# Kernel tuning notes

Hardware: AMD Instinct MI355X
Metric: run time of the kernel (lower is better)

## Reference

```python
import jax, jax.numpy as jnp
import numpy as np

DIM = 1024
FF = 4096
E = 8
K = 2


def setup_inputs() -> dict:
    key = jax.random.key(0)
    ks = jax.random.split(key, 6)
    x = jax.random.normal(ks[0], (4, 2048, DIM), dtype=jnp.float32)
    wr = jax.random.normal(ks[1], (E, DIM), dtype=jnp.float32) * 0.02   # router weight [E, D]
    w1 = jax.random.normal(ks[2], (E, DIM, 2 * FF), dtype=jnp.float32) * 0.02  # SwiGLU in-proj
    b1 = jax.random.normal(ks[3], (E, 2 * FF), dtype=jnp.float32) * 0.02
    w2 = jax.random.normal(ks[4], (E, FF, DIM), dtype=jnp.float32) * 0.02  # SwiGLU out-proj
    b2 = jax.random.normal(ks[5], (E, DIM), dtype=jnp.float32) * 0.02
    return {"x": x, "wr": wr, "w1": w1, "b1": b1, "w2": w2, "b2": b2}


def reference(x, wr, w1, b1, w2, b2):
    B, T, D = x.shape
    n_experts = wr.shape[0]
    xf = x.reshape(B * T, D)                      # [N, D]
    logits = xf @ wr.T                            # [N, E]
    topk_vals, topk_idx = jax.lax.top_k(logits, K)  # [N, K]
    gates = jax.nn.softmax(topk_vals, axis=-1)      # [N, K]
    out = jnp.zeros_like(xf)
    for e in range(n_experts):
        # combined gate weight for tokens routed to expert e (0 otherwise)
        g_e = jnp.sum(jnp.where(topk_idx == e, gates, 0.0), axis=-1)  # [N]
        u = xf @ w1[e] + b1[e]                    # [N, 2F]
        a, b = jnp.split(u, 2, axis=-1)
        h = jax.nn.silu(a) * b                    # SwiGLU
        y_e = h @ w2[e] + b2[e]                   # [N, D]
        out = out + g_e[:, None] * y_e
    return out.reshape(B, T, D)
```

## Files before the change

kernel.cpp:

```cpp
#include <hip/hip_runtime.h>

#define NE 8
#define NTOK 8192
#define NDIM 1024
#define NFF 4096

typedef short bf16x8 __attribute__((ext_vector_type(8)));
typedef float f32x4 __attribute__((ext_vector_type(4)));
typedef unsigned short us_t;
typedef us_t us4 __attribute__((ext_vector_type(4)));
typedef us_t us8 __attribute__((ext_vector_type(8)));

#define MFMA16 __builtin_amdgcn_mfma_f32_16x16x32_bf16

__device__ __forceinline__ us_t f2bf(float f) {
  unsigned int u = __float_as_uint(f);
  u += 0x7fffu + ((u >> 16) & 1u);
  return (us_t)(u >> 16);
}

__device__ __forceinline__ void gload16(const void* g, void* l) {
  __builtin_amdgcn_global_load_lds(
      (const __attribute__((address_space(1))) void*)g,
      (__attribute__((address_space(3))) void*)l, 16, 0, 0);
}

__global__ __launch_bounds__(256) void router_kernel(
    const float* __restrict__ x, const float* __restrict__ wr,
    int* __restrict__ counts, int* __restrict__ tok_list,
    int4* __restrict__ tok4, float2* __restrict__ gate2,
    us_t* __restrict__ xbf)
{
  __shared__ float wr_s[NE * NDIM];
  int tid = threadIdx.x;
#pragma unroll
  for (int i = 0; i < 8; ++i)
    ((float4*)wr_s)[tid + 256 * i] = ((const float4*)wr)[tid + 256 * i];
  __syncthreads();
  int w = tid >> 6, l = tid & 63;
  int t = blockIdx.x * 4 + w;
  float4 xv[4];
#pragma unroll
  for (int j = 0; j < 4; ++j) xv[j] = ((const float4*)x)[(size_t)t * 256 + j * 64 + l];
#pragma unroll
  for (int j = 0; j < 4; ++j) {
    us4 o;
    o.x = f2bf(xv[j].x); o.y = f2bf(xv[j].y); o.z = f2bf(xv[j].z); o.w = f2bf(xv[j].w);
    ((us4*)xbf)[(size_t)t * 256 + j * 64 + l] = o;
  }
  float logits[NE];
#pragma unroll
  for (int e = 0; e < NE; ++e) {
    float p = 0.f;
#pragma unroll
    for (int j = 0; j < 4; ++j) {
      float4 wv = ((const float4*)wr_s)[e * 256 + j * 64 + l];
      p += xv[j].x * wv.x + xv[j].y * wv.y + xv[j].z * wv.z + xv[j].w * wv.w;
    }
#pragma unroll
    for (int s = 32; s > 0; s >>= 1) p += __shfl_xor(p, s, 64);
    logits[e] = p;
  }
  if (l == 0) {
    int e1 = 0; float v1 = logits[0];
#pragma unroll
    for (int e = 1; e < NE; ++e) if (logits[e] > v1) { v1 = logits[e]; e1 = e; }
    int e2 = -1; float v2 = -3.4e38f;
#pragma unroll
    for (int e = 0; e < NE; ++e) if (e != e1 && logits[e] > v2) { v2 = logits[e]; e2 = e; }
    float ge = expf(v2 - v1);
    float g1 = 1.f / (1.f + ge);
    float g2 = 1.f - g1;
    int i1 = atomicAdd(&counts[e1], 1);
    tok_list[e1 * NTOK + i1] = t;
    int i2 = atomicAdd(&counts[e2], 1);
    tok_list[e2 * NTOK + i2] = t;
    tok4[t] = make_int4(e1, i1, e2, i2);
    gate2[t] = make_float2(g1, g2);
  }
}

__global__ void prefix8(const int* __restrict__ counts, int* __restrict__ offsets) {
  if (threadIdx.x == 0) {
    int s = 0;
    for (int e = 0; e < NE; ++e) { offsets[e] = s; s += counts[e]; }
  }
}

__global__ __launch_bounds__(256) void transpose_cvt(
    const float* __restrict__ in, us_t* __restrict__ out, int R, int C)
{
  __shared__ float tile[64][65];
  int e = blockIdx.z;
  const float* ip = in + (size_t)e * R * C;
  us_t* op = out + (size_t)e * R * C;
  int r0 = blockIdx.y * 64, c0 = blockIdx.x * 64;
  int tid = threadIdx.x;
#pragma unroll
  for (int q = 0; q < 4; ++q) {
    int id = tid + 256 * q;
    int rr = id >> 4, c4 = id & 15;
    float4 v = *(const float4*)&ip[(size_t)(r0 + rr) * C + c0 + c4 * 4];
    tile[rr][c4 * 4 + 0] = v.x; tile[rr][c4 * 4 + 1] = v.y;
    tile[rr][c4 * 4 + 2] = v.z; tile[rr][c4 * 4 + 3] = v.w;
  }
  __syncthreads();
#pragma unroll
  for (int q = 0; q < 2; ++q) {
    int id = tid + 256 * q;
    int cc = id >> 3, r8 = id & 7;
    us8 o;
#pragma unroll
    for (int j = 0; j < 8; ++j) o[j] = f2bf(tile[r8 * 8 + j][cc]);
    *(us8*)&op[(size_t)(c0 + cc) * R + r0 + r8 * 8] = o;
  }
}

__global__ __launch_bounds__(256) void gemm1_swiglu(
    const us_t* __restrict__ xbf,
    const us_t* __restrict__ w1T,
    const float* __restrict__ b1,
    const int* __restrict__ counts, const int* __restrict__ offsets,
    const int* __restrict__ tok_list,
    us_t* __restrict__ hbuf)
{
  const int e = blockIdx.z, mt = blockIdx.y, ct = blockIdx.x;
  const int cnt = counts[e];
  if (mt * 128 >= cnt) return;
  const int off = offsets[e];
  const int tid = threadIdx.x, w = tid >> 6, l = tid & 63;
  const int wr_ = w >> 1, wc = w & 1;

  __shared__ char ldsA[16384];
  __shared__ char ldsB[32768];
  __shared__ int tok_l[128];

  if (tid < 128) {
    int r = mt * 128 + tid;
    tok_l[tid] = tok_list[e * NTOK + (r < cnt ? r : cnt - 1)];
  }
  __syncthreads();

  f32x4 zf = {0.f, 0.f, 0.f, 0.f};
  f32x4 acc[2][4][4];
#pragma unroll
  for (int h_ = 0; h_ < 2; ++h_)
#pragma unroll
    for (int cg = 0; cg < 4; ++cg)
#pragma unroll
      for (int rg = 0; rg < 4; ++rg) acc[h_][cg][rg] = zf;

  const size_t w1base = (size_t)e * 2 * NFF * NDIM;

  for (int kt = 0; kt < NDIM; kt += 64) {
    __syncthreads();
#pragma unroll
    for (int i = 0; i < 12; ++i) {
      int c = w + i * 4;
      const us_t* gsrc; char* ldst;
      if (c < 16) {
        int p = c * 1024 + l * 16;
        int row = p >> 7;
        int ir = (p & 127) ^ ((row & 7) << 4);
        gsrc = xbf + (size_t)tok_l[row] * NDIM + kt + (ir >> 1);
        ldst = ldsA + c * 1024;
      } else {
        int cb = c - 16;
        int p = cb * 1024 + l * 16;
        int row = p >> 7;
        int ir = (p & 127) ^ ((row & 7) << 4);
        int ncol = (row < 128) ? (ct * 128 + row) : (NFF + ct * 128 + row - 128);
        gsrc = w1T + w1base + (size_t)ncol * NDIM + kt + (ir >> 1);
        ldst = ldsB + cb * 1024;
      }
      gload16(gsrc, ldst);
    }
    __syncthreads();
#pragma unroll
    for (int ks = 0; ks < 2; ++ks) {
      bf16x8 af[4];
#pragma unroll
      for (int rg = 0; rg < 4; ++rg) {
        int row = wr_ * 64 + rg * 16 + (l & 15);
        int ir = (ks * 64 + (l >> 4) * 16) ^ ((row & 7) << 4);
        af[rg] = *(const bf16x8*)(ldsA + row * 128 + ir);
      }
#pragma unroll
      for (int h_ = 0; h_ < 2; ++h_)
#pragma unroll
        for (int cg = 0; cg < 4; ++cg) {
          int crow = h_ * 128 + wc * 64 + cg * 16 + (l & 15);
          int ir = (ks * 64 + (l >> 4) * 16) ^ ((crow & 7) << 4);
          bf16x8 bfr = *(const bf16x8*)(ldsB + crow * 128 + ir);
#pragma unroll
          for (int rg = 0; rg < 4; ++rg)
            acc[h_][cg][rg] = MFMA16(af[rg], bfr, acc[h_][cg][rg], 0, 0, 0);
        }
    }
  }

  float b1a[4], b1b[4];
#pragma unroll
  for (int cg = 0; cg < 4; ++cg) {
    int n_a = ct * 128 + wc * 64 + cg * 16 + (l & 15);
    b1a[cg] = b1[e * 2 * NFF + n_a];
    b1b[cg] = b1[e * 2 * NFF + NFF + n_a];
  }
#pragma unroll
  for (int cg = 0; cg < 4; ++cg) {
    int n_a = ct * 128 + wc * 64 + cg * 16 + (l & 15);
#pragma unroll
    for (int rg = 0; rg < 4; ++rg) {
#pragma unroll
      for (int j = 0; j < 4; ++j) {
        int rt = wr_ * 64 + rg * 16 + (l >> 4) * 4 + j;
        int r = mt * 128 + rt;
        if (r < cnt) {
          float a = acc[0][cg][rg][j] + b1a[cg];
          float b = acc[1][cg][rg][j] + b1b[cg];
          float hv = (a / (1.f + __expf(-a))) * b;
          hbuf[(size_t)(off + r) * NFF + n_a] = f2bf(hv);
        }
      }
    }
  }
}

__global__ __launch_bounds__(256) void gemm2_slot(
    const us_t* __restrict__ hbuf,
    const us_t* __restrict__ w2T,
    const float* __restrict__ b2,
    const int* __restrict__ counts, const int* __restrict__ offsets,
    float* __restrict__ ybuf)
{
  const int b = blockIdx.x;
  const int xcd = b & 7, k = b >> 3;
  const int mt = k & 63;
  const int combo = xcd + 8 * (k >> 6);
  const int nt = combo & 7, e = combo >> 3;

  const int cnt = counts[e];
  if (mt * 128 >= cnt) return;
  const int off = offsets[e];
  const int tid = threadIdx.x, w = tid >> 6, l = tid & 63;
  const int wr_ = w >> 1, wc = w & 1;

  __shared__ char ldsA[16384];
  __shared__ char ldsB[16384];

  unsigned int soff[8];
#pragma unroll
  for (int i = 0; i < 8; ++i) {
    int c = w + i * 4;
    if (i < 4) {
      int p = c * 1024 + l * 16;
      int row = p >> 7;
      int ir = (p & 127) ^ ((row & 7) << 4);
      int r = mt * 128 + row; if (r >= cnt) r = cnt - 1;
      soff[i] = (unsigned int)((off + r) * (NFF * 2) + ir);
    } else {
      int cb = c - 16;
      int p = cb * 1024 + l * 16;
      int row = p >> 7;
      int ir = (p & 127) ^ ((row & 7) << 4);
      soff[i] = (unsigned int)((nt * 128 + row) * (NFF * 2) + ir);
    }
  }

  f32x4 zf = {0.f, 0.f, 0.f, 0.f};
  f32x4 acc[4][4];
#pragma unroll
  for (int cg = 0; cg < 4; ++cg)
#pragma unroll
    for (int rg = 0; rg < 4; ++rg) acc[cg][rg] = zf;

  const char* hB = (const char*)hbuf;
  const char* wB = (const char*)w2T + (size_t)e * NDIM * NFF * 2;

  for (int ktb = 0; ktb < NFF * 2; ktb += 128) {
    __syncthreads();
#pragma unroll
    for (int i = 0; i < 4; ++i)
      gload16(hB + soff[i] + ktb, ldsA + (w + i * 4) * 1024);
#pragma unroll
    for (int i = 4; i < 8; ++i)
      gload16(wB + soff[i] + ktb, ldsB + (w + i * 4 - 16) * 1024);
    __syncthreads();
#pragma unroll
    for (int ks = 0; ks < 2; ++ks) {
      bf16x8 af[4];
#pragma unroll
      for (int rg = 0; rg < 4; ++rg) {
        int row = wr_ * 64 + rg * 16 + (l & 15);
        int ir = (ks * 64 + (l >> 4) * 16) ^ ((row & 7) << 4);
        af[rg] = *(const bf16x8*)(ldsA + row * 128 + ir);
      }
#pragma unroll
      for (int cg = 0; cg < 4; ++cg) {
        int crow = wc * 64 + cg * 16 + (l & 15);
        int ir = (ks * 64 + (l >> 4) * 16) ^ ((crow & 7) << 4);
        bf16x8 bfr = *(const bf16x8*)(ldsB + crow * 128 + ir);
#pragma unroll
        for (int rg = 0; rg < 4; ++rg)
          acc[cg][rg] = MFMA16(af[rg], bfr, acc[cg][rg], 0, 0, 0);
      }
    }
  }

#pragma unroll
  for (int cg = 0; cg < 4; ++cg) {
    int col = nt * 128 + wc * 64 + cg * 16 + (l & 15);
    float b2v = b2[e * NDIM + col];
#pragma unroll
    for (int rg = 0; rg < 4; ++rg) {
#pragma unroll
      for (int j = 0; j < 4; ++j) {
        int rt = wr_ * 64 + rg * 16 + (l >> 4) * 4 + j;
        int r = mt * 128 + rt;
        if (r < cnt)
          ybuf[(size_t)(off + r) * NDIM + col] = acc[cg][rg][j] + b2v;
      }
    }
  }
}

__global__ __launch_bounds__(256) void combine_kernel(
    const float* __restrict__ ybuf, const int* __restrict__ offsets,
    const int4* __restrict__ tok4, const float2* __restrict__ gate2,
    float* __restrict__ out)
{
  int t = blockIdx.x;
  int4 p = tok4[t];
  float2 g = gate2[t];
  int s1 = offsets[p.x] + p.y;
  int s2 = offsets[p.z] + p.w;
  const float4* y1 = (const float4*)(ybuf + (size_t)s1 * NDIM);
  const float4* y2 = (const float4*)(ybuf + (size_t)s2 * NDIM);
  float4 a = y1[threadIdx.x];
  float4 b = y2[threadIdx.x];
  float4 o;
  o.x = g.x * a.x + g.y * b.x;
  o.y = g.x * a.y + g.y * b.y;
  o.z = g.x * a.z + g.y * b.z;
  o.w = g.x * a.w + g.y * b.w;
  ((float4*)(out + (size_t)t * NDIM))[threadIdx.x] = o;
}

extern "C" void kernel_launch(void* const* d_in, const int* in_sizes, int n_in,
                              void* d_out, int out_size, void* d_ws, size_t ws_size,
                              hipStream_t stream) {
  const float* x  = (const float*)d_in[0];
  const float* wr = (const float*)d_in[1];
  const float* w1 = (const float*)d_in[2];
  const float* b1 = (const float*)d_in[3];
  const float* w2 = (const float*)d_in[4];
  const float* b2 = (const float*)d_in[5];
  float* out = (float*)d_out;
  char* ws = (char*)d_ws;

  int*    counts   = (int*)(ws + 0);
  int*    offsets  = (int*)(ws + 256);
  int*    tok_list = (int*)(ws + 512);
  int4*   tok4     = (int4*)(ws + 512 + 262144);
  float2* gate2    = (float2*)(ws + 512 + 262144 + 131072);
  us_t*   xbf      = (us_t*)(ws + 524800);
  us_t*   hbuf     = (us_t*)(ws + 524800 + (size_t)NTOK * NDIM * 2);
  us_t*   wT       = (us_t*)(ws + 524800 + (size_t)NTOK * NDIM * 2
                                          + (size_t)2 * NTOK * NFF * 2);
  float*  ybuf     = (float*)((char*)wT + 67108864);

  hipMemsetAsync(counts, 0, 32, stream);

  router_kernel<<<NTOK / 4, 256, 0, stream>>>(x, wr, counts, tok_list, tok4, gate2, xbf);
  prefix8<<<1, 64, 0, stream>>>(counts, offsets);

  transpose_cvt<<<dim3(2 * NFF / 64, NDIM / 64, NE), 256, 0, stream>>>(w1, wT, NDIM, 2 * NFF);
  gemm1_swiglu<<<dim3(NFF / 128, NTOK / 128, NE), 256, 0, stream>>>(
      xbf, wT, b1, counts, offsets, tok_list, hbuf);

  transpose_cvt<<<dim3(NDIM / 64, NFF / 64, NE), 256, 0, stream>>>(w2, wT, NFF, NDIM);
  gemm2_slot<<<4096, 256, 0, stream>>>(
      hbuf, wT, b2, counts, offsets, ybuf);

  combine_kernel<<<NTOK, 256, 0, stream>>>(ybuf, offsets, tok4, gate2, out);
}
```

Measured before the change: 958.2 us.

## Split gemm2 K dimension in two with atomic accumulation and move bias to combine

Splits the second expert GEMM along the FF reduction dimension into two halves, doubling the grid and accumulating partial results into ybuf with float atomicAdd. ybuf is zeroed with a memset beforehand, and the b2 bias add moves into the combine kernel. The aim is more parallel blocks for better CU occupancy, at the cost of a large memset, atomic write traffic and nondeterministic summation order.

```diff
diff --git a/kernel.cpp b/kernel.cpp
--- a/kernel.cpp
+++ b/kernel.cpp
@@ -229,7 +229,6 @@
 __global__ __launch_bounds__(256) void gemm2_slot(
     const us_t* __restrict__ hbuf,
     const us_t* __restrict__ w2T,
-    const float* __restrict__ b2,
     const int* __restrict__ counts, const int* __restrict__ offsets,
     float* __restrict__ ybuf)
 {
@@ -237,7 +236,9 @@
   const int xcd = b & 7, k = b >> 3;
   const int mt = k & 63;
   const int combo = xcd + 8 * (k >> 6);
-  const int nt = combo & 7, e = combo >> 3;
+  const int nt = combo & 7;
+  const int ks = (combo >> 3) & 1;
+  const int e = combo >> 4;
 
   const int cnt = counts[e];
   if (mt * 128 >= cnt) return;
@@ -277,7 +278,8 @@
   const char* hB = (const char*)hbuf;
   const char* wB = (const char*)w2T + (size_t)e * NDIM * NFF * 2;
 
-  for (int ktb = 0; ktb < NFF * 2; ktb += 128) {
+  const int ktb0 = ks * 4096;
+  for (int ktb = ktb0; ktb < ktb0 + 4096; ktb += 128) {
     __syncthreads();
 #pragma unroll
     for (int i = 0; i < 4; ++i)
@@ -287,18 +289,18 @@
       gload16(wB + soff[i] + ktb, ldsB + (w + i * 4 - 16) * 1024);
     __syncthreads();
 #pragma unroll
-    for (int ks = 0; ks < 2; ++ks) {
+    for (int ks2 = 0; ks2 < 2; ++ks2) {
       bf16x8 af[4];
 #pragma unroll
       for (int rg = 0; rg < 4; ++rg) {
         int row = wr_ * 64 + rg * 16 + (l & 15);
-        int ir = (ks * 64 + (l >> 4) * 16) ^ ((row & 7) << 4);
+        int ir = (ks2 * 64 + (l >> 4) * 16) ^ ((row & 7) << 4);
         af[rg] = *(const bf16x8*)(ldsA + row * 128 + ir);
       }
 #pragma unroll
       for (int cg = 0; cg < 4; ++cg) {
         int crow = wc * 64 + cg * 16 + (l & 15);
-        int ir = (ks * 64 + (l >> 4) * 16) ^ ((crow & 7) << 4);
+        int ir = (ks2 * 64 + (l >> 4) * 16) ^ ((crow & 7) << 4);
         bf16x8 bfr = *(const bf16x8*)(ldsB + crow * 128 + ir);
 #pragma unroll
         for (int rg = 0; rg < 4; ++rg)
@@ -310,7 +312,6 @@
 #pragma unroll
   for (int cg = 0; cg < 4; ++cg) {
     int col = nt * 128 + wc * 64 + cg * 16 + (l & 15);
-    float b2v = b2[e * NDIM + col];
 #pragma unroll
     for (int rg = 0; rg < 4; ++rg) {
 #pragma unroll
@@ -318,7 +319,7 @@
         int rt = wr_ * 64 + rg * 16 + (l >> 4) * 4 + j;
         int r = mt * 128 + rt;
         if (r < cnt)
-          ybuf[(size_t)(off + r) * NDIM + col] = acc[cg][rg][j] + b2v;
+          atomicAdd(&ybuf[(size_t)(off + r) * NDIM + col], acc[cg][rg][j]);
       }
     }
   }
@@ -327,22 +328,22 @@
 __global__ __launch_bounds__(256) void combine_kernel(
     const float* __restrict__ ybuf, const int* __restrict__ offsets,
     const int4* __restrict__ tok4, const float2* __restrict__ gate2,
-    float* __restrict__ out)
+    const float* __restrict__ b2, float* __restrict__ out)
 {
   int t = blockIdx.x;
   int4 p = tok4[t];
   float2 g = gate2[t];
   int s1 = offsets[p.x] + p.y;
   int s2 = offsets[p.z] + p.w;
-  const float4* y1 = (const float4*)(ybuf + (size_t)s1 * NDIM);
-  const float4* y2 = (const float4*)(ybuf + (size_t)s2 * NDIM);
-  float4 a = y1[threadIdx.x];
-  float4 b = y2[threadIdx.x];
+  float4 a = ((const float4*)(ybuf + (size_t)s1 * NDIM))[threadIdx.x];
+  float4 b = ((const float4*)(ybuf + (size_t)s2 * NDIM))[threadIdx.x];
+  float4 ba = ((const float4*)(b2 + (size_t)p.x * NDIM))[threadIdx.x];
+  float4 bb = ((const float4*)(b2 + (size_t)p.z * NDIM))[threadIdx.x];
   float4 o;
-  o.x = g.x * a.x + g.y * b.x;
-  o.y = g.x * a.y + g.y * b.y;
-  o.z = g.x * a.z + g.y * b.z;
-  o.w = g.x * a.w + g.y * b.w;
+  o.x = g.x * (a.x + ba.x) + g.y * (b.x + bb.x);
+  o.y = g.x * (a.y + ba.y) + g.y * (b.y + bb.y);
+  o.z = g.x * (a.z + ba.z) + g.y * (b.z + bb.z);
+  o.w = g.x * (a.w + ba.w) + g.y * (b.w + bb.w);
   ((float4*)(out + (size_t)t * NDIM))[threadIdx.x] = o;
 }
 
@@ -378,9 +379,11 @@
   gemm1_swiglu<<<dim3(NFF / 128, NTOK / 128, NE), 256, 0, stream>>>(
       xbf, wT, b1, counts, offsets, tok_list, hbuf);
 
+  hipMemsetAsync(ybuf, 0, (size_t)2 * NTOK * NDIM * sizeof(float), stream);
+
   transpose_cvt<<<dim3(NDIM / 64, NFF / 64, NE), 256, 0, stream>>>(w2, wT, NFF, NDIM);
-  gemm2_slot<<<4096, 256, 0, stream>>>(
-      hbuf, wT, b2, counts, offsets, ybuf);
-
-  combine_kernel<<<NTOK, 256, 0, stream>>>(ybuf, offsets, tok4, gate2, out);
-}
+  gemm2_slot<<<8192, 256, 0, stream>>>(
+      hbuf, wT, counts, offsets, ybuf);
+
+  combine_kernel<<<NTOK, 256, 0, stream>>>(ybuf, offsets, tok4, gate2, b2, out);
+}
```

Result: slower. 980.6 us (+2.3%).
